# Kernel optimization log

Measured on AMD Instinct MI355X. Metric: run time of the kernel, lower is better.

## Reference

```python
import jax, jax.numpy as jnp
import numpy as np

NUM_ATTRS = 8    # A: number of attribute names in attr_map
NUM_VALS = 16    # V: number of distinct values per attribute


def setup_inputs() -> dict:
    key = jax.random.key(0)
    k1, k2 = jax.random.split(key)
    B, D = 2_000_000, 8
    predictions = jax.random.normal(k1, (B, D), dtype=jnp.float32)
    attr_vals = jax.random.randint(k2, (B, NUM_ATTRS), 0, NUM_VALS, dtype=jnp.int32)
    return {"predictions": predictions, "attr_vals": attr_vals}


def reference(predictions, attr_vals):
    B, A = attr_vals.shape
    V = NUM_VALS
    # per-node mean of sigmoid probs; stacking rows then .mean() == mean of per-node means
    per_node = jnp.mean(jax.nn.sigmoid(predictions), axis=1)  # [B]
    # flatten (attr, value) groups into A*V segments
    seg_ids = (attr_vals + jnp.arange(A, dtype=attr_vals.dtype)[None, :] * V).reshape(-1)  # [B*A]
    vals = jnp.broadcast_to(per_node[:, None], (B, A)).reshape(-1)  # [B*A]
    sums = jax.ops.segment_sum(vals, seg_ids, num_segments=A * V)
    counts = jax.ops.segment_sum(jnp.ones_like(vals), seg_ids, num_segments=A * V)
    means = (sums / jnp.maximum(counts, 1.0)).reshape(A, V)      # [A, V]
    present = (counts > 0).reshape(A, V)                          # [A, V]
    # pairwise squared diffs of group means within each attribute (i < j)
    diff = means[:, :, None] - means[:, None, :]                  # [A, V, V]
    triu = jnp.triu(jnp.ones((V, V), dtype=bool), k=1)
    pair_mask = present[:, :, None] & present[:, None, :] & triu[None, :, :]
    total_loss = jnp.sum(jnp.where(pair_mask, diff * diff, 0.0))
    num_comparisons = jnp.sum(pair_mask)
    return jnp.where(num_comparisons > 0, total_loss / num_comparisons, 0.0)
```

## Files before the change

### kernel.cpp

```cpp
#include <hip/hip_runtime.h>

#define NA 8
#define NV 16
#define NS (NA * NV)
#define NW 4
#define FIX_SHIFT 43
#define FIX_MASK ((1ULL << FIX_SHIFT) - 1)
#define FIX_SCALE 16384.0f
#define CNT_SH 23
#define CELL_MASK ((1u << CNT_SH) - 1)


__device__ __forceinline__ float sig(float x) {
    return __builtin_amdgcn_rcpf(1.0f + __expf(-x));
}

__device__ __forceinline__ void process_chunk(
    float4 p, int4 a, int lane, unsigned int* __restrict__ hw)
{
    float hs = sig(p.x) + sig(p.y) + sig(p.z) + sig(p.w);
    float s  = hs + __shfl_xor(hs, 1, 64);
    unsigned int fixed = (unsigned int)(s * 2048.0f);
    unsigned int add   = (1u << CNT_SH) | fixed;
    const int abase = (lane & 1) << 2;
    atomicAdd(&hw[((abase + 0) << 4) + a.x], add);
    atomicAdd(&hw[((abase + 1) << 4) + a.y], add);
    atomicAdd(&hw[((abase + 2) << 4) + a.z], add);
    atomicAdd(&hw[((abase + 3) << 4) + a.w], add);
}

__global__ __launch_bounds__(256) void k1_accum(
    const float* __restrict__ preds,
    const int*   __restrict__ attrs,
    unsigned long long* __restrict__ partials,
    int B, int nb)
{
    __shared__ unsigned int h[NW][NS];
    for (int i = threadIdx.x; i < NW * NS; i += 256)
        ((unsigned int*)h)[i] = 0u;
    __syncthreads();

    const int lane = threadIdx.x & 63;
    const int wave = threadIdx.x >> 6;
    unsigned int* __restrict__ hw = h[wave];

    const float4* __restrict__ p4 = (const float4*)preds;
    const int4*   __restrict__ a4 = (const int4*)attrs;

    const int gw      = blockIdx.x * NW + wave;
    const int nwv     = nb * NW;
    const int nchunks = B >> 5;

    int c = gw;
    if (c < nchunks) {
        float4 p = p4[(size_t)c * 64 + lane];
        int4   a = a4[(size_t)c * 64 + lane];
        for (;;) {
            const int  cn   = c + nwv;
            const bool more = (cn < nchunks);
            float4 pn; int4 an;
            if (more) {
                pn = p4[(size_t)cn * 64 + lane];
                an = a4[(size_t)cn * 64 + lane];
            }
            process_chunk(p, a, lane, hw);
            if (!more) break;
            p = pn; a = an; c = cn;
        }
    }

    const int rem = B & 31;
    if (rem && blockIdx.x == 0 && wave == 0 && lane < rem * 2) {
        const size_t base = (size_t)(B >> 5) * 64;
        float4 p = p4[base + lane];
        int4   a = a4[base + lane];
        process_chunk(p, a, lane, hw);
    }
    __syncthreads();

    if (threadIdx.x < NS) {
        unsigned long long cnt = 0ULL, fix = 0ULL;
        #pragma unroll
        for (int w = 0; w < NW; ++w) {
            unsigned int cell = h[w][threadIdx.x];
            cnt += (cell >> CNT_SH);
            fix += (cell & CELL_MASK);
        }
        partials[(size_t)threadIdx.x * nb + blockIdx.x] =
            (cnt << FIX_SHIFT) | fix;
    }
}

__global__ __launch_bounds__(256) void k2_reduce(
    const unsigned long long* __restrict__ partials,
    double* __restrict__ means,
    int*    __restrict__ pres,
    int nb)
{
    const int s = blockIdx.x;
    unsigned long long sum = 0ULL;
    unsigned int cnt = 0u;
    for (int b = threadIdx.x; b < nb; b += 256) {
        unsigned long long p = partials[(size_t)s * nb + b];
        cnt += (unsigned int)(p >> FIX_SHIFT);
        sum += (p & FIX_MASK);
    }
    for (int off = 32; off > 0; off >>= 1) {
        sum += __shfl_down(sum, off, 64);
        cnt += __shfl_down(cnt, off, 64);
    }
    __shared__ unsigned long long ws_[4];
    __shared__ unsigned int wc_[4];
    const int wave = threadIdx.x >> 6;
    if ((threadIdx.x & 63) == 0) { ws_[wave] = sum; wc_[wave] = cnt; }
    __syncthreads();
    if (threadIdx.x == 0) {
        unsigned long long S = ws_[0] + ws_[1] + ws_[2] + ws_[3];
        unsigned int C = wc_[0] + wc_[1] + wc_[2] + wc_[3];
        means[s] = C ? ((double)S * (1.0 / (double)FIX_SCALE)) / (double)C : 0.0;
        pres[s]  = C ? 1 : 0;
    }
}

__global__ __launch_bounds__(128) void k3_finalize(
    const double* __restrict__ means,
    const int*    __restrict__ pres,
    float* __restrict__ out)
{
    __shared__ double s_mean[NS];
    __shared__ int    s_pres[NS];
    const int t = threadIdx.x;
    s_mean[t] = means[t];
    s_pres[t] = pres[t];
    __syncthreads();

    const int a = t >> 4;
    const int i = t & (NV - 1);
    double loss = 0.0;
    int    ncmp = 0;
    if (s_pres[t]) {
        const double mi = s_mean[t];
        for (int j = i + 1; j < NV; ++j) {
            const int sj = a * NV + j;
            if (s_pres[sj]) {
                const double d = mi - s_mean[sj];
                loss += d * d;
                ncmp += 1;
            }
        }
    }
    for (int off = 32; off > 0; off >>= 1) {
        loss += __shfl_down(loss, off, 64);
        ncmp += __shfl_down(ncmp, off, 64);
    }
    __shared__ double w_loss[2];
    __shared__ int    w_ncmp[2];
    const int wave = t >> 6;
    if ((t & 63) == 0) { w_loss[wave] = loss; w_ncmp[wave] = ncmp; }
    __syncthreads();
    if (t == 0) {
        const double total = w_loss[0] + w_loss[1];
        const int    n     = w_ncmp[0] + w_ncmp[1];
        out[0] = (n > 0) ? (float)(total / (double)n) : 0.0f;
    }
}

extern "C" void kernel_launch(void* const* d_in, const int* in_sizes, int n_in,
                              void* d_out, int out_size, void* d_ws, size_t ws_size,
                              hipStream_t stream) {
    const float* preds = (const float*)d_in[0];
    const int*   attrs = (const int*)d_in[1];
    float*       out   = (float*)d_out;

    const int B = in_sizes[1] / NA;

    const size_t tail = NS * sizeof(double) + NS * sizeof(int);
    int nb = 2048;
    if (ws_size < (size_t)NS * nb * sizeof(unsigned long long) + tail) nb = 1024;

    unsigned long long* partials = (unsigned long long*)d_ws;
    double* means = (double*)((char*)d_ws + (size_t)NS * nb * sizeof(unsigned long long));
    int*    pres  = (int*)(means + NS);

    k1_accum<<<nb, 256, 0, stream>>>(preds, attrs, partials, B, nb);
    k2_reduce<<<NS, 256, 0, stream>>>(partials, means, pres, nb);
    k3_finalize<<<1, 128, 0, stream>>>(means, pres, out);
}
```

Baseline: 153.9 us.

## Replace LDS atomic histograms with per-lane register accumulators and wave shuffles

Each lane keeps a 4x16 register histogram updated by predicated compare-adds instead of LDS atomicAdds, then reduces across the wave with xor shuffles and writes per-wave partials. This removes LDS atomic contention and block syncs. In exchange it uses many more VGPRs and ALU ops, writes four times more partials for the second kernel to read, and lowers the fixed-point scale to fit a narrower value field, reducing precision.

```diff
diff --git a/kernel.cpp b/kernel.cpp
--- a/kernel.cpp
+++ b/kernel.cpp
@@ -6,27 +6,13 @@
 #define NW 4
 #define FIX_SHIFT 43
 #define FIX_MASK ((1ULL << FIX_SHIFT) - 1)
-#define FIX_SCALE 16384.0f
-#define CNT_SH 23
+#define FIX_SCALE_D 4096.0
+#define CNT_SH 22
 #define CELL_MASK ((1u << CNT_SH) - 1)
 
 
 __device__ __forceinline__ float sig(float x) {
     return __builtin_amdgcn_rcpf(1.0f + __expf(-x));
-}
-
-__device__ __forceinline__ void process_chunk(
-    float4 p, int4 a, int lane, unsigned int* __restrict__ hw)
-{
-    float hs = sig(p.x) + sig(p.y) + sig(p.z) + sig(p.w);
-    float s  = hs + __shfl_xor(hs, 1, 64);
-    unsigned int fixed = (unsigned int)(s * 2048.0f);
-    unsigned int add   = (1u << CNT_SH) | fixed;
-    const int abase = (lane & 1) << 2;
-    atomicAdd(&hw[((abase + 0) << 4) + a.x], add);
-    atomicAdd(&hw[((abase + 1) << 4) + a.y], add);
-    atomicAdd(&hw[((abase + 2) << 4) + a.z], add);
-    atomicAdd(&hw[((abase + 3) << 4) + a.w], add);
 }
 
 __global__ __launch_bounds__(256) void k1_accum(
@@ -35,20 +21,20 @@
     unsigned long long* __restrict__ partials,
     int B, int nb)
 {
-    __shared__ unsigned int h[NW][NS];
-    for (int i = threadIdx.x; i < NW * NS; i += 256)
-        ((unsigned int*)h)[i] = 0u;
-    __syncthreads();
-
     const int lane = threadIdx.x & 63;
     const int wave = threadIdx.x >> 6;
-    unsigned int* __restrict__ hw = h[wave];
+    const int gw   = blockIdx.x * NW + wave;
+    const int nwv  = nb * NW;
+
+    unsigned int acc[4][16];
+    #pragma unroll
+    for (int k = 0; k < 4; ++k)
+        #pragma unroll
+        for (int j = 0; j < 16; ++j) acc[k][j] = 0u;
 
     const float4* __restrict__ p4 = (const float4*)preds;
     const int4*   __restrict__ a4 = (const int4*)attrs;
 
-    const int gw      = blockIdx.x * NW + wave;
-    const int nwv     = nb * NW;
     const int nchunks = B >> 5;
 
     int c = gw;
@@ -63,7 +49,18 @@
                 pn = p4[(size_t)cn * 64 + lane];
                 an = a4[(size_t)cn * 64 + lane];
             }
-            process_chunk(p, a, lane, hw);
+            {
+                float hs = sig(p.x) + sig(p.y) + sig(p.z) + sig(p.w);
+                float s  = hs + __shfl_xor(hs, 1, 64);
+                unsigned int add = (1u << CNT_SH) | (unsigned int)(s * 512.0f);
+                #pragma unroll
+                for (int j = 0; j < 16; ++j) {
+                    acc[0][j] += (a.x == j) ? add : 0u;
+                    acc[1][j] += (a.y == j) ? add : 0u;
+                    acc[2][j] += (a.z == j) ? add : 0u;
+                    acc[3][j] += (a.w == j) ? add : 0u;
+                }
+            }
             if (!more) break;
             p = pn; a = an; c = cn;
         }
@@ -74,20 +71,35 @@
         const size_t base = (size_t)(B >> 5) * 64;
         float4 p = p4[base + lane];
         int4   a = a4[base + lane];
-        process_chunk(p, a, lane, hw);
-    }
-    __syncthreads();
-
-    if (threadIdx.x < NS) {
-        unsigned long long cnt = 0ULL, fix = 0ULL;
+        float hs = sig(p.x) + sig(p.y) + sig(p.z) + sig(p.w);
+        float s  = hs + __shfl_xor(hs, 1, 64);
+        unsigned int add = (1u << CNT_SH) | (unsigned int)(s * 512.0f);
         #pragma unroll
-        for (int w = 0; w < NW; ++w) {
-            unsigned int cell = h[w][threadIdx.x];
-            cnt += (cell >> CNT_SH);
-            fix += (cell & CELL_MASK);
-        }
-        partials[(size_t)threadIdx.x * nb + blockIdx.x] =
-            (cnt << FIX_SHIFT) | fix;
+        for (int j = 0; j < 16; ++j) {
+            acc[0][j] += (a.x == j) ? add : 0u;
+            acc[1][j] += (a.y == j) ? add : 0u;
+            acc[2][j] += (a.z == j) ? add : 0u;
+            acc[3][j] += (a.w == j) ? add : 0u;
+        }
+    }
+
+    #pragma unroll
+    for (int k = 0; k < 4; ++k) {
+        #pragma unroll
+        for (int j = 0; j < 16; ++j) {
+            unsigned int t = acc[k][j];
+            t += __shfl_xor(t, 2, 64);
+            t += __shfl_xor(t, 4, 64);
+            t += __shfl_xor(t, 8, 64);
+            t += __shfl_xor(t, 16, 64);
+            t += __shfl_xor(t, 32, 64);
+            if (lane < 2) {
+                const int seg = (k + ((lane & 1) << 2)) * NV + j;
+                partials[(size_t)seg * nwv + gw] =
+                    ((unsigned long long)(t >> CNT_SH) << FIX_SHIFT)
+                    | (unsigned long long)(t & CELL_MASK);
+            }
+        }
     }
 }
 
@@ -95,13 +107,13 @@
     const unsigned long long* __restrict__ partials,
     double* __restrict__ means,
     int*    __restrict__ pres,
-    int nb)
+    int ncol)
 {
     const int s = blockIdx.x;
     unsigned long long sum = 0ULL;
     unsigned int cnt = 0u;
-    for (int b = threadIdx.x; b < nb; b += 256) {
-        unsigned long long p = partials[(size_t)s * nb + b];
+    for (int b = threadIdx.x; b < ncol; b += 256) {
+        unsigned long long p = partials[(size_t)s * ncol + b];
         cnt += (unsigned int)(p >> FIX_SHIFT);
         sum += (p & FIX_MASK);
     }
@@ -117,7 +129,7 @@
     if (threadIdx.x == 0) {
         unsigned long long S = ws_[0] + ws_[1] + ws_[2] + ws_[3];
         unsigned int C = wc_[0] + wc_[1] + wc_[2] + wc_[3];
-        means[s] = C ? ((double)S * (1.0 / (double)FIX_SCALE)) / (double)C : 0.0;
+        means[s] = C ? ((double)S * (1.0 / FIX_SCALE_D)) / (double)C : 0.0;
         pres[s]  = C ? 1 : 0;
     }
 }
@@ -176,13 +188,16 @@
 
     const size_t tail = NS * sizeof(double) + NS * sizeof(int);
     int nb = 2048;
-    if (ws_size < (size_t)NS * nb * sizeof(unsigned long long) + tail) nb = 1024;
+    if (ws_size < (size_t)NS * nb * NW * sizeof(unsigned long long) + tail)
+        nb = 1024;
+    const int ncol = nb * NW;
 
     unsigned long long* partials = (unsigned long long*)d_ws;
-    double* means = (double*)((char*)d_ws + (size_t)NS * nb * sizeof(unsigned long long));
+    double* means = (double*)((char*)d_ws +
+                              (size_t)NS * ncol * sizeof(unsigned long long));
     int*    pres  = (int*)(means + NS);
 
     k1_accum<<<nb, 256, 0, stream>>>(preds, attrs, partials, B, nb);
-    k2_reduce<<<NS, 256, 0, stream>>>(partials, means, pres, nb);
+    k2_reduce<<<NS, 256, 0, stream>>>(partials, means, pres, ncol);
     k3_finalize<<<1, 128, 0, stream>>>(means, pres, out);
 }
```

Result: slower. 180.9 us (+17.6%).

## Fuse finalize into reduce via last-block counter and split LDS histograms per half-wave

Applied to the files above, without the earlier changes.

Removes the third kernel launch by having the last k2 block, found through an agent-scope atomic counter reset in k1, compute the pairwise loss. Separately, each wave's shared histogram is split into two copies keyed by half-wave, which is meant to cut LDS atomic contention on the shared bins. Costs are twice the LDS histogram footprint and the release/acquire atomics in k2.

```diff
diff --git a/kernel.cpp b/kernel.cpp
--- a/kernel.cpp
+++ b/kernel.cpp
@@ -4,9 +4,10 @@
 #define NV 16
 #define NS (NA * NV)
 #define NW 4
+#define NR 2
 #define FIX_SHIFT 43
 #define FIX_MASK ((1ULL << FIX_SHIFT) - 1)
-#define FIX_SCALE 16384.0f
+#define FIX_SCALE_D 16384.0
 #define CNT_SH 23
 #define CELL_MASK ((1u << CNT_SH) - 1)
 
@@ -33,16 +34,20 @@
     const float* __restrict__ preds,
     const int*   __restrict__ attrs,
     unsigned long long* __restrict__ partials,
+    int* __restrict__ counter,
     int B, int nb)
 {
-    __shared__ unsigned int h[NW][NS];
-    for (int i = threadIdx.x; i < NW * NS; i += 256)
+    __shared__ unsigned int h[NW][NR][NS];
+    for (int i = threadIdx.x; i < NW * NR * NS; i += 256)
         ((unsigned int*)h)[i] = 0u;
+    if (blockIdx.x == 0 && threadIdx.x == 0)
+        __hip_atomic_store(counter, 0, __ATOMIC_RELAXED,
+                           __HIP_MEMORY_SCOPE_AGENT);
     __syncthreads();
 
     const int lane = threadIdx.x & 63;
     const int wave = threadIdx.x >> 6;
-    unsigned int* __restrict__ hw = h[wave];
+    unsigned int* __restrict__ hw = h[wave][lane >> 5];
 
     const float4* __restrict__ p4 = (const float4*)preds;
     const int4*   __restrict__ a4 = (const int4*)attrs;
@@ -81,20 +86,24 @@
     if (threadIdx.x < NS) {
         unsigned long long cnt = 0ULL, fix = 0ULL;
         #pragma unroll
-        for (int w = 0; w < NW; ++w) {
-            unsigned int cell = h[w][threadIdx.x];
-            cnt += (cell >> CNT_SH);
-            fix += (cell & CELL_MASK);
-        }
+        for (int w = 0; w < NW; ++w)
+            #pragma unroll
+            for (int r = 0; r < NR; ++r) {
+                unsigned int cell = h[w][r][threadIdx.x];
+                cnt += (cell >> CNT_SH);
+                fix += (cell & CELL_MASK);
+            }
         partials[(size_t)threadIdx.x * nb + blockIdx.x] =
             (cnt << FIX_SHIFT) | fix;
     }
 }
 
-__global__ __launch_bounds__(256) void k2_reduce(
+__global__ __launch_bounds__(256) void k2_reduce_finalize(
     const unsigned long long* __restrict__ partials,
     double* __restrict__ means,
     int*    __restrict__ pres,
+    int*    __restrict__ counter,
+    float*  __restrict__ out,
     int nb)
 {
     const int s = blockIdx.x;
@@ -114,31 +123,39 @@
     const int wave = threadIdx.x >> 6;
     if ((threadIdx.x & 63) == 0) { ws_[wave] = sum; wc_[wave] = cnt; }
     __syncthreads();
+
+    __shared__ int lastFlag;
     if (threadIdx.x == 0) {
         unsigned long long S = ws_[0] + ws_[1] + ws_[2] + ws_[3];
         unsigned int C = wc_[0] + wc_[1] + wc_[2] + wc_[3];
-        means[s] = C ? ((double)S * (1.0 / (double)FIX_SCALE)) / (double)C : 0.0;
-        pres[s]  = C ? 1 : 0;
-    }
-}
-
-__global__ __launch_bounds__(128) void k3_finalize(
-    const double* __restrict__ means,
-    const int*    __restrict__ pres,
-    float* __restrict__ out)
-{
+        double m = C ? ((double)S * (1.0 / FIX_SCALE_D)) / (double)C : 0.0;
+        __hip_atomic_store(&means[s], m, __ATOMIC_RELEASE,
+                           __HIP_MEMORY_SCOPE_AGENT);
+        __hip_atomic_store(&pres[s], C ? 1 : 0, __ATOMIC_RELEASE,
+                           __HIP_MEMORY_SCOPE_AGENT);
+        int old = __hip_atomic_fetch_add(counter, 1, __ATOMIC_ACQ_REL,
+                                         __HIP_MEMORY_SCOPE_AGENT);
+        lastFlag = (old == NS - 1);
+    }
+    __syncthreads();
+    if (!lastFlag) return;
+
     __shared__ double s_mean[NS];
     __shared__ int    s_pres[NS];
     const int t = threadIdx.x;
-    s_mean[t] = means[t];
-    s_pres[t] = pres[t];
-    __syncthreads();
-
-    const int a = t >> 4;
-    const int i = t & (NV - 1);
+    if (t < NS) {
+        s_mean[t] = __hip_atomic_load(&means[t], __ATOMIC_ACQUIRE,
+                                      __HIP_MEMORY_SCOPE_AGENT);
+        s_pres[t] = __hip_atomic_load(&pres[t], __ATOMIC_ACQUIRE,
+                                      __HIP_MEMORY_SCOPE_AGENT);
+    }
+    __syncthreads();
+
     double loss = 0.0;
     int    ncmp = 0;
-    if (s_pres[t]) {
+    if (t < NS && s_pres[t]) {
+        const int a = t >> 4;
+        const int i = t & (NV - 1);
         const double mi = s_mean[t];
         for (int j = i + 1; j < NV; ++j) {
             const int sj = a * NV + j;
@@ -153,14 +170,13 @@
         loss += __shfl_down(loss, off, 64);
         ncmp += __shfl_down(ncmp, off, 64);
     }
-    __shared__ double w_loss[2];
-    __shared__ int    w_ncmp[2];
-    const int wave = t >> 6;
+    __shared__ double w_loss[4];
+    __shared__ int    w_ncmp[4];
     if ((t & 63) == 0) { w_loss[wave] = loss; w_ncmp[wave] = ncmp; }
     __syncthreads();
     if (t == 0) {
-        const double total = w_loss[0] + w_loss[1];
-        const int    n     = w_ncmp[0] + w_ncmp[1];
+        const double total = w_loss[0] + w_loss[1] + w_loss[2] + w_loss[3];
+        const int    n     = w_ncmp[0] + w_ncmp[1] + w_ncmp[2] + w_ncmp[3];
         out[0] = (n > 0) ? (float)(total / (double)n) : 0.0f;
     }
 }
@@ -174,15 +190,17 @@
 
     const int B = in_sizes[1] / NA;
 
-    const size_t tail = NS * sizeof(double) + NS * sizeof(int);
+    const size_t tail = NS * sizeof(double) + NS * sizeof(int) + sizeof(int);
     int nb = 2048;
     if (ws_size < (size_t)NS * nb * sizeof(unsigned long long) + tail) nb = 1024;
 
     unsigned long long* partials = (unsigned long long*)d_ws;
-    double* means = (double*)((char*)d_ws + (size_t)NS * nb * sizeof(unsigned long long));
-    int*    pres  = (int*)(means + NS);
-
-    k1_accum<<<nb, 256, 0, stream>>>(preds, attrs, partials, B, nb);
-    k2_reduce<<<NS, 256, 0, stream>>>(partials, means, pres, nb);
-    k3_finalize<<<1, 128, 0, stream>>>(means, pres, out);
-}
+    double* means = (double*)((char*)d_ws +
+                              (size_t)NS * nb * sizeof(unsigned long long));
+    int*    pres    = (int*)(means + NS);
+    int*    counter = pres + NS;
+
+    k1_accum<<<nb, 256, 0, stream>>>(preds, attrs, partials, counter, B, nb);
+    k2_reduce_finalize<<<NS, 256, 0, stream>>>(partials, means, pres,
+                                               counter, out, nb);
+}
```

After: 156.3 us. Within noise of the previous version (+1.6%).
